# Kernel tuning notes

Measured on AMD Instinct MI355X. Metric: run time of the kernel, lower is better.

Reference implementation:

```python
import jax, jax.numpy as jnp
import numpy as np
from jax import lax

K = 4
OUT_PLANES = 128
TEMPERATURE = 30.0


def setup_inputs() -> dict:
    key = jax.random.key(0)
    ks = jax.random.split(key, 5)
    in_planes, k = 128, 3
    he_std = float(np.sqrt(2.0)) * (in_planes * k * k) ** (-0.5)
    return {
        "x": jax.random.normal(ks[0], (16, in_planes, 64, 64), jnp.float32),
        "weight": jax.random.normal(ks[1], (K * OUT_PLANES, in_planes, k, k), jnp.float32) * he_std,
        "bias": jax.random.normal(ks[2], (K * OUT_PLANES,), jnp.float32) * 0.01,
        "se_w1": jax.random.normal(ks[3], (33, in_planes), jnp.float32) * (2.0 / 33) ** 0.5,
        "se_w2": jax.random.normal(ks[4], (K, 33), jnp.float32) * (2.0 / K) ** 0.5,
        "se_b2": jnp.zeros((K,), jnp.float32),
    }


def reference(x, weight, bias, se_w1, se_w2, se_b2):
    B = x.shape[0]
    # SE attention: global avg pool -> fc1 -> relu -> fc2 -> softmax(./T)
    pooled = x.mean(axis=(2, 3))                      # [B, Cin]
    h = jax.nn.relu(pooled @ se_w1.T)                 # [B, hidden]
    logits = h @ se_w2.T + se_b2                      # [B, K]
    attn = jax.nn.softmax(logits / TEMPERATURE, axis=1)
    # conv with K*out channels (groups=1, stride=1, pad=1, dil=1)
    y = lax.conv_general_dilated(
        x, weight, window_strides=(1, 1), padding=[(1, 1), (1, 1)],
        dimension_numbers=("NCHW", "OIHW", "NCHW"))
    y = y + bias[None, :, None, None]                 # [B, K*out, Ho, Wo]
    Ho, Wo = y.shape[2], y.shape[3]
    y = y.reshape(B, K, OUT_PLANES, Ho, Wo)
    # attention-weighted combine over K branches (bmm in torch)
    return jnp.einsum("bk,bkohw->bohw", attn, y)
```

## Files before the change

### kernel.cpp

```cpp
#include <hip/hip_runtime.h>
#include <cstdint>
#include <cstddef>

typedef unsigned short u16;
typedef __attribute__((ext_vector_type(8))) short short8;
typedef __attribute__((ext_vector_type(4))) float f32x4;

__device__ __forceinline__ u16 f2bf(float f){
  union { float f; unsigned u; } c; c.f = f;
  unsigned u = c.u;
  u += 0x7fffu + ((u >> 16) & 1u);
  return (u16)(u >> 16);
}
__device__ __forceinline__ unsigned pk2(float a, float b){
  union { float f; unsigned u; } ca, cb; ca.f = a; cb.f = b;
  return ((ca.u + 0x8000u) >> 16) | ((cb.u + 0x8000u) & 0xFFFF0000u);
}

#define XB_STRIDE 557568
#define XR_STRIDE 8448


#define GLD_LDS(gsrc, ldst) \
  __builtin_amdgcn_global_load_lds((const __attribute__((address_space(1))) void*)(gsrc), \
                                   (__attribute__((address_space(3))) void*)(ldst), 16, 0, 0)

#define BAR { asm volatile("s_waitcnt lgkmcnt(0)" ::: "memory"); \
              __builtin_amdgcn_s_barrier(); }
#define WAIT_VM(N) asm volatile("s_waitcnt vmcnt(" #N ")" ::: "memory")

__global__ __launch_bounds__(256) void xpose_pool(
    const float* __restrict__ x, u16* __restrict__ xT2, float* __restrict__ part)
{
  const int bid = blockIdx.x;
  const int b = bid & 15, chunk = bid >> 4;
  const int pos0 = chunk << 6;
  const int tid = threadIdx.x;
  __shared__ u16 tile[8192];
  __shared__ float psum[128 * 17];
  const float* xb = x + ((size_t)b << 19) + pos0;
  const int rq = tid & 15;
  const int p4 = rq << 2;
  const int gci = tid >> 4;

  if (chunk == 0){
    u16* xh = xT2 + (size_t)b * XB_STRIDE;
    for (int i = tid; i < 4160; i += 256){
      const int p = i >> 4, oct = i & 15;
      int row, col;
      if (p < 66)      { row = 0;        col = p; }
      else if (p < 132){ row = 65;       col = p - 66; }
      else if (p < 196){ row = p - 131;  col = 0; }
      else             { row = p - 195;  col = 65; }
      *(uint4*)(xh + row * XR_STRIDE + (col << 7) + (oct << 3)) =
          make_uint4(0u, 0u, 0u, 0u);
    }
  }

  {
    const int ci8 = gci << 3;
    float4 L[8];
    #pragma unroll
    for (int j = 0; j < 8; ++j)
      L[j] = *(const float4*)(xb + ((size_t)(ci8 + j) << 12) + p4);
    #pragma unroll
    for (int j = 0; j < 8; ++j)
      psum[(ci8 + j) * 17 + rq] = L[j].x + L[j].y + L[j].z + L[j].w;
    const int gs = gci ^ (rq & 7);
    const float* e = (const float*)L;
    #pragma unroll
    for (int p = 0; p < 4; ++p){
      const int row = p4 + p;
      uint4 V;
      V.x = pk2(e[0 * 4 + p], e[1 * 4 + p]);
      V.y = pk2(e[2 * 4 + p], e[3 * 4 + p]);
      V.z = pk2(e[4 * 4 + p], e[5 * 4 + p]);
      V.w = pk2(e[6 * 4 + p], e[7 * 4 + p]);
      *(uint4*)(tile + (row << 7) + (gs << 3)) = V;
    }
  }
  __syncthreads();

  if (tid < 128){
    float s = 0.f;
    #pragma unroll
    for (int j = 0; j < 16; ++j) s += psum[tid * 17 + j];
    part[(((b << 6) | chunk) << 7) + tid] = s;
  }

  u16* xo = xT2 + (size_t)b * XB_STRIDE;
  const int g = tid & 15, rb = (tid >> 4) << 2;
  #pragma unroll
  for (int r = 0; r < 4; ++r){
    const int row = rb + r;
    const int gs = g ^ ((row >> 2) & 7);
    uint4 v = *(const uint4*)(tile + (row << 7) + (gs << 3));
    const int pos = pos0 + row;
    const int h = pos >> 6, w = pos & 63;
    *(uint4*)(xo + (h + 1) * XR_STRIDE + ((w + 1) << 7) + (g << 3)) = v;
  }
}

__global__ __launch_bounds__(256) void combine(
    const float* __restrict__ W, const float* __restrict__ bias,
    const float* __restrict__ part, const float* __restrict__ w1,
    const float* __restrict__ w2, const float* __restrict__ b2,
    u16* __restrict__ wcomb, float* __restrict__ bcomb)
{
  __shared__ float wlds[9216];
  __shared__ float sp[128];
  __shared__ float sh[33];
  __shared__ float sat[4];
  const int bid = blockIdx.x;
  const int b = bid & 15, cp = bid >> 4;
  const int tid = threadIdx.x;

  #pragma unroll
  for (int it = 0; it < 9; ++it){
    const int G = it * 256 + tid;
    const int k = G / 576, rem = G - k * 576;
    const int co_l = rem / 288, j4 = rem - co_l * 288;
    const float* src = W + (size_t)(k * 128 + (cp << 1) + co_l) * 1152 + (j4 << 2);
    GLD_LDS(src, (char*)wlds + (G << 4));
  }

  if (tid < 128){
    const float* pb = part + (b << 13);
    float s = 0.f;
    #pragma unroll 8
    for (int c = 0; c < 64; ++c) s += pb[(c << 7) + tid];
    sp[tid] = s * (1.f / 4096.f);
  }
  __syncthreads();
  if (tid < 33){
    float h = 0.f;
    for (int ci = 0; ci < 128; ++ci) h += sp[ci] * w1[tid * 128 + ci];
    sh[tid] = fmaxf(h, 0.f);
  }
  __syncthreads();
  if (tid == 0){
    float l[4];
    #pragma unroll
    for (int t = 0; t < 4; ++t){
      float v = b2[t];
      for (int j = 0; j < 33; ++j) v += sh[j] * w2[t * 33 + j];
      l[t] = v * (1.f / 30.f);
    }
    float m = fmaxf(fmaxf(l[0], l[1]), fmaxf(l[2], l[3]));
    float e0 = __expf(l[0] - m), e1 = __expf(l[1] - m);
    float e2 = __expf(l[2] - m), e3 = __expf(l[3] - m);
    float inv = 1.f / (e0 + e1 + e2 + e3);
    sat[0] = e0 * inv; sat[1] = e1 * inv; sat[2] = e2 * inv; sat[3] = e3 * inv;
  }
  asm volatile("s_waitcnt vmcnt(0)" ::: "memory");
  __syncthreads();
  const float a0 = sat[0], a1 = sat[1], a2 = sat[2], a3 = sat[3];

  if (tid < 2){
    const int co = (cp << 1) + tid;
    bcomb[(b << 7) + co] = a0 * bias[co] + a1 * bias[128 + co]
                         + a2 * bias[256 + co] + a3 * bias[384 + co];
  }

  u16* wob = wcomb + (size_t)b * 147456;
  for (int gi = tid; gi < 288; gi += 256){
    const int co_l = gi / 144;
    const int r = gi - co_l * 144;
    const int tap = r >> 4;
    const int gg = r & 15;
    const int q = gg >> 2, g = gg & 3;
    const int co = (cp << 1) + co_l;
    union { u16 h[8]; uint4 v; } pk;
    #pragma unroll
    for (int e = 0; e < 8; ++e){
      const int ci = (q << 5) + (g << 3) + e;
      const int j = ci * 9 + tap;
      float s = a0 * wlds[co_l * 1152 + j]        + a1 * wlds[2304 + co_l * 1152 + j]
              + a2 * wlds[4608 + co_l * 1152 + j] + a3 * wlds[6912 + co_l * 1152 + j];
      pk.h[e] = f2bf(s);
    }
    *(uint4*)(wob + (((tap << 2) + q) << 12) + (co << 5) + (g << 3)) = pk.v;
  }
}

__global__ __launch_bounds__(256, 2) void conv_mfma(
    const u16* __restrict__ xT2, const u16* __restrict__ wcomb,
    const float* __restrict__ bcomb, float* __restrict__ out)
{
  extern __shared__ char smem[];
  u16* s_x = (u16*)smem;
  u16* s_w = (u16*)(smem + 33792);

  const int tid = threadIdx.x;
  const int lane = tid & 63, wid = tid >> 6;
  const int wr = wid & 1, wcv = wid >> 1;
  const int l15 = lane & 15, hi = lane >> 4;

  const int bid = blockIdx.x;
  const int b = bid & 15;
  const int h0 = (bid >> 4) << 1;

  const u16* Abase = wcomb + (size_t)b * 147456;
  const u16* Xbase = xT2 + (size_t)b * XB_STRIDE;

#define STAGE_X(Q) { \
    u16* _sx = s_x + ((Q) & 1) * 8448; \
    _Pragma("unroll") \
    for (int _it = 0; _it < 5; ++_it){ \
      const int _G = _it * 256 + tid; \
      if (_it < 4 || _G < 1056){ \
        const int _oct = _G & 3, _t = _G >> 2; \
        const int _col = _t % 66, _row = _t / 66; \
        const u16* _src = Xbase + (h0 + _row) * XR_STRIDE + (_col << 7) \
                        + ((Q) << 5) + (_oct << 3); \
        GLD_LDS(_src, _sx + (_G << 3)); \
      } \
    } }

#define STAGE_W(Q, TAP, BUF) { \
    const u16* _As = Abase + ((((TAP) << 2) + (Q)) << 12); \
    u16* _sw = s_w + (BUF) * 4096; \
    GLD_LDS(_As + (tid << 3), _sw + (tid << 3)); \
    GLD_LDS(_As + ((tid + 256) << 3), _sw + ((tid + 256) << 3)); }

#define COMPUTE(Q, TAP, BUF) { \
    const int _dh = (TAP) / 3, _dw = (TAP) - 3 * (_dh); \
    const u16* _sw = s_w + (BUF) * 4096; \
    const u16* _sx = s_x + ((Q) & 1) * 8448; \
    short8 _af[4], _bf[4]; \
    _Pragma("unroll") \
    for (int _a = 0; _a < 4; ++_a){ \
      const int _co = (wcv << 6) + (_a << 4) + l15; \
      _af[_a] = *(const short8*)(_sw + (_co << 5) + (hi << 3)); \
    } \
    _Pragma("unroll") \
    for (int _p = 0; _p < 4; ++_p){ \
      const int _col = l15 + _dw + (_p << 4); \
      _bf[_p] = *(const short8*)(_sx + (((wr + _dh) * 66 + _col) << 5) + (hi << 3)); \
    } \
    _Pragma("unroll") \
    for (int _a = 0; _a < 4; ++_a) \
      _Pragma("unroll") \
      for (int _p = 0; _p < 4; ++_p) \
        acc[_a][_p] = __builtin_amdgcn_mfma_f32_16x16x32_bf16(_af[_a], _bf[_p], acc[_a][_p], 0, 0, 0); }

  f32x4 acc[4][4] = {};

  STAGE_X(0);
  STAGE_W(0, 0, 0);
  STAGE_W(0, 1, 1);

  for (int q = 0; q < 4; ++q){
    #pragma unroll
    for (int tap = 0; tap < 9; ++tap){
      if (q == 3 && tap == 8)                  { WAIT_VM(0); }
      else if (q < 3 && (tap == 6 || tap == 7)){ WAIT_VM(6); }
      else                                     { WAIT_VM(2); }
      BAR;
      if (tap <= 6){
        STAGE_W(q, tap + 2, (tap + 2) % 3);
      } else if (tap == 7){
        if (q < 3){ STAGE_W(q + 1, 0, 0); }
      } else {
        if (q < 3){ STAGE_W(q + 1, 1, 1); }
      }
      if (tap == 5 && q < 3){ STAGE_X(q + 1); }
      __builtin_amdgcn_s_setprio(1);
      COMPUTE(q, tap, tap % 3);
      __builtin_amdgcn_s_setprio(0);
    }
  }

#undef COMPUTE
#undef STAGE_W
#undef STAGE_X

  const int hrow = h0 + wr;
  float* ob = out + ((size_t)b << 19) + (hrow << 6) + l15;
  #pragma unroll
  for (int a = 0; a < 4; ++a){
    const int co0 = (wcv << 6) + (a << 4) + (hi << 2);
    #pragma unroll
    for (int r = 0; r < 4; ++r){
      const float bc = bcomb[(b << 7) + co0 + r];
      float* op = ob + (size_t)(co0 + r) * 4096;
      #pragma unroll
      for (int p = 0; p < 4; ++p)
        __builtin_nontemporal_store(acc[a][p][r] + bc, op + (p << 4));
    }
  }
}

extern "C" void kernel_launch(void* const* d_in, const int* in_sizes, int n_in,
                              void* d_out, int out_size, void* d_ws, size_t ws_size,
                              hipStream_t stream)
{
  const float* x    = (const float*)d_in[0];
  const float* W    = (const float*)d_in[1];
  const float* bias = (const float*)d_in[2];
  const float* w1   = (const float*)d_in[3];
  const float* w2   = (const float*)d_in[4];
  const float* b2   = (const float*)d_in[5];
  float* out = (float*)d_out;

  char* ws = (char*)d_ws;
  float* part  = (float*)(ws);
  float* bcomb = (float*)(ws + 524288);
  u16*   xT2   = (u16*)  (ws + 532480);
  u16*   wcomb = (u16*)  (ws + 18374656);

  xpose_pool<<<1024, 256, 0, stream>>>(x, xT2, part);
  combine<<<1024, 256, 0, stream>>>(W, bias, part, w1, w2, b2, wcomb, bcomb);

  (void)hipFuncSetAttribute(reinterpret_cast<const void*>(conv_mfma),
                            hipFuncAttributeMaxDynamicSharedMemorySize, 58368);
  conv_mfma<<<512, 256, 58368, stream>>>(xT2, wcomb, bcomb, out);
}
```

Baseline: 49.33 us.

## Give each wave a private double-buffered weight slice and drop per-tap barriers

Each wave now stages only the 64-output-channel weight slice it consumes into its own double-buffered LDS region. This lets the per-tap block-wide barriers go away, leaving one barrier per channel quarter to cover the shared x tile. The aim is to remove synchronization stalls between waves in the tap loop. In exchange, weight loads are duplicated across waves that share the same channel group, and LDS per block grows to 66560 bytes, which may limit occupancy.

```diff
diff --git a/kernel.cpp b/kernel.cpp
--- a/kernel.cpp
+++ b/kernel.cpp
@@ -218,20 +218,23 @@
     } }
 
 #define STAGE_W(Q, TAP, BUF) { \
-    const u16* _As = Abase + ((((TAP) << 2) + (Q)) << 12); \
-    u16* _sw = s_w + (BUF) * 4096; \
-    GLD_LDS(_As + (tid << 3), _sw + (tid << 3)); \
-    GLD_LDS(_As + ((tid + 256) << 3), _sw + ((tid + 256) << 3)); }
+    const u16* _As = Abase + ((((TAP) << 2) + (Q)) << 12) + (wcv << 11); \
+    u16* _sw = s_w + (wid << 12) + ((BUF) << 11); \
+    _Pragma("unroll") \
+    for (int _it = 0; _it < 4; ++_it){ \
+      const int _g = (_it << 6) + lane; \
+      GLD_LDS(_As + (_g << 3), _sw + (_g << 3)); \
+    } }
 
 #define COMPUTE(Q, TAP, BUF) { \
     const int _dh = (TAP) / 3, _dw = (TAP) - 3 * (_dh); \
-    const u16* _sw = s_w + (BUF) * 4096; \
+    const u16* _sw = s_w + (wid << 12) + ((BUF) << 11); \
     const u16* _sx = s_x + ((Q) & 1) * 8448; \
     short8 _af[4], _bf[4]; \
     _Pragma("unroll") \
     for (int _a = 0; _a < 4; ++_a){ \
-      const int _co = (wcv << 6) + (_a << 4) + l15; \
-      _af[_a] = *(const short8*)(_sw + (_co << 5) + (hi << 3)); \
+      const int _cl = (_a << 4) + l15; \
+      _af[_a] = *(const short8*)(_sw + (_cl << 5) + (hi << 3)); \
     } \
     _Pragma("unroll") \
     for (int _p = 0; _p < 4; ++_p){ \
@@ -248,26 +251,26 @@
 
   STAGE_X(0);
   STAGE_W(0, 0, 0);
-  STAGE_W(0, 1, 1);
+  WAIT_VM(0);
+  __syncthreads();
 
   for (int q = 0; q < 4; ++q){
     #pragma unroll
     for (int tap = 0; tap < 9; ++tap){
-      if (q == 3 && tap == 8)                  { WAIT_VM(0); }
-      else if (q < 3 && (tap == 6 || tap == 7)){ WAIT_VM(6); }
-      else                                     { WAIT_VM(2); }
-      BAR;
-      if (tap <= 6){
-        STAGE_W(q, tap + 2, (tap + 2) % 3);
-      } else if (tap == 7){
-        if (q < 3){ STAGE_W(q + 1, 0, 0); }
-      } else {
-        if (q < 3){ STAGE_W(q + 1, 1, 1); }
+      const int s = q * 9 + tap;
+      if (s < 35){
+        const int nq = (tap == 8) ? q + 1 : q;
+        const int nt = (tap == 8) ? 0 : tap + 1;
+        STAGE_W(nq, nt, (s + 1) & 1);
       }
       if (tap == 5 && q < 3){ STAGE_X(q + 1); }
+      if (s == 35)                             { WAIT_VM(0); }
+      else if (q < 3 && (tap == 5 || tap == 6)){ WAIT_VM(8); }
+      else                                     { WAIT_VM(4); }
       __builtin_amdgcn_s_setprio(1);
-      COMPUTE(q, tap, tap % 3);
+      COMPUTE(q, tap, s & 1);
       __builtin_amdgcn_s_setprio(0);
+      if (tap == 8 && q < 3){ BAR; }
     }
   }
 
@@ -313,6 +316,6 @@
   combine<<<1024, 256, 0, stream>>>(W, bias, part, w1, w2, b2, wcomb, bcomb);
 
   (void)hipFuncSetAttribute(reinterpret_cast<const void*>(conv_mfma),
-                            hipFuncAttributeMaxDynamicSharedMemorySize, 58368);
-  conv_mfma<<<512, 256, 58368, stream>>>(xT2, wcomb, bcomb, out);
-}
+                            hipFuncAttributeMaxDynamicSharedMemorySize, 66560);
+  conv_mfma<<<512, 256, 66560, stream>>>(xT2, wcomb, bcomb, out);
+}
```

New measurement: 49.61 us. About the same (+0.6%).
